# Kernel optimization log

Measured on AMD Instinct MI355X. Metric: run time of the kernel, lower is better.

The kernel has to match this reference:

```python
import jax, jax.numpy as jnp
import numpy as np

H = 12      # num_attention_heads
DM = 768    # hidden_size
HD = DM // H  # head_dim = 64


def setup_inputs() -> dict:
    key = jax.random.key(0)
    ks = jax.random.split(key, 9)
    B, L = 4, 2048
    s = 0.02
    return {
        "hidden_states": jax.random.normal(ks[0], (B, L, DM), jnp.float32),
        "wq": jax.random.normal(ks[1], (DM, DM), jnp.float32) * s,
        "bq": jnp.zeros((DM,), jnp.float32),
        "wk": jax.random.normal(ks[2], (DM, DM), jnp.float32) * s,
        "bk": jnp.zeros((DM,), jnp.float32),
        "wv": jax.random.normal(ks[3], (DM, DM), jnp.float32) * s,
        "bv": jnp.zeros((DM,), jnp.float32),
        "wo": jax.random.normal(ks[4], (DM, DM), jnp.float32) * s,
        "bo": jnp.zeros((DM,), jnp.float32),
    }


def reference(hidden_states, wq, bq, wk, bk, wv, bv, wo, bo):
    B, L, D = hidden_states.shape
    scale = HD ** -0.5
    # torch Linear: x @ W.T + b
    q = hidden_states @ wq.T + bq
    k = hidden_states @ wk.T + bk
    v = hidden_states @ wv.T + bv
    # [B, H, L, HD]
    q = q.reshape(B, L, H, HD).transpose(0, 2, 1, 3)
    k = k.reshape(B, L, H, HD).transpose(0, 2, 1, 3)
    v = v.reshape(B, L, H, HD).transpose(0, 2, 1, 3)
    attn = jnp.einsum('bhqd,bhkd->bhqk', q, k) * scale
    causal = jnp.tril(jnp.ones((L, L), dtype=bool))
    attn = jnp.where(causal, attn, jnp.float32(-jnp.inf))
    attn = jax.nn.softmax(attn, axis=-1)
    out = jnp.einsum('bhqk,bhkd->bhqd', attn, v)
    out = out.transpose(0, 2, 1, 3).reshape(B, L, D)
    return out @ wo.T + bo
```

## Files before the change

kernel.cpp:

```cpp
#include <hip/hip_runtime.h>

typedef unsigned short ushort_t;
typedef __attribute__((ext_vector_type(8))) short short8;
typedef __attribute__((ext_vector_type(4))) float f32x4;

__device__ __forceinline__ ushort_t f2b(float f) {
    union { float f; unsigned int i; } v; v.f = f;
    unsigned int x = v.i;
    return (ushort_t)((x + 0x7fffu + ((x >> 16) & 1u)) >> 16);
}
__device__ __forceinline__ ushort_t f2b_fast(float f) {
    union { float f; unsigned int i; } v; v.f = f;
    return (ushort_t)((v.i + 0x8000u) >> 16);
}
__device__ __forceinline__ float exp2_hw(float x) {
    return __builtin_amdgcn_exp2f(x);
}
__device__ __forceinline__ void dma16(const ushort_t* g, ushort_t* l) {
    __builtin_amdgcn_global_load_lds(
        (const __attribute__((address_space(1))) unsigned int*)g,
        (__attribute__((address_space(3))) unsigned int*)l, 16, 0, 0);
}

__global__ __launch_bounds__(256)
void convert_bf16(const float* __restrict__ hs, const float* __restrict__ wq,
                  const float* __restrict__ wk, const float* __restrict__ wv,
                  const float* __restrict__ wo,
                  ushort_t* __restrict__ hsb, ushort_t* __restrict__ wqb,
                  ushort_t* __restrict__ wkb, ushort_t* __restrict__ wvb,
                  ushort_t* __restrict__ wob)
{
    const int y = blockIdx.y;
    const float* src; ushort_t* dst; int n;
    if (y == 0)      { src = hs; dst = hsb; n = 8192 * 768; }
    else if (y == 1) { src = wq; dst = wqb; n = 768 * 768; }
    else if (y == 2) { src = wk; dst = wkb; n = 768 * 768; }
    else if (y == 3) { src = wv; dst = wvb; n = 768 * 768; }
    else             { src = wo; dst = wob; n = 768 * 768; }
    const int idx = (blockIdx.x * 256 + threadIdx.x) * 8;
    if (idx >= n) return;
    const float4 a = ((const float4*)(src + idx))[0];
    const float4 b = ((const float4*)(src + idx))[1];
    ushort_t tmp[8] = { f2b(a.x), f2b(a.y), f2b(a.z), f2b(a.w),
                        f2b(b.x), f2b(b.y), f2b(b.z), f2b(b.w) };
    *(uint4*)(dst + idx) = *(const uint4*)tmp;
}

#define NIT 24

template<int MODE>
__global__ __launch_bounds__(256, 3)
void gemm_mfma(const ushort_t* __restrict__ A,
               const ushort_t* __restrict__ W0, const ushort_t* __restrict__ W1,
               const ushort_t* __restrict__ W2,
               const float* __restrict__ b0, const float* __restrict__ b1,
               const float* __restrict__ b2,
               void* __restrict__ C0, void* __restrict__ C1, void* __restrict__ C2)
{
    __shared__ __attribute__((aligned(16))) ushort_t Ab[3][128 * 32];
    __shared__ __attribute__((aligned(16))) ushort_t Wb[3][128 * 32];

    const int id   = blockIdx.x;
    const int xcd  = id & 7;
    const int slot = id >> 3;
    int mtile, otile, z;
    if (MODE == 0) {
        mtile = (slot / 18) * 8 + xcd;
        const int rem = slot % 18;
        otile = rem % 6;
        z     = rem / 6;
    } else {
        mtile = (slot / 6) * 8 + xcd;
        otile = slot % 6;
        z     = 0;
    }
    const ushort_t* W = (z == 0) ? W0 : (z == 1) ? W1 : W2;
    const float* bias  = (z == 0) ? b0 : (z == 1) ? b1 : b2;
    void* C            = (z == 0) ? C0 : (z == 1) ? C1 : C2;

    const int t    = threadIdx.x;
    const int lane = t & 63;
    const int w    = t >> 6;
    const int col  = lane & 15;
    const int kg   = lane >> 4;
    const int m0   = mtile * 128;
    const int o0   = otile * 128;
    const int mh   = (w & 1) * 64;
    const int oh   = (w >> 1) * 64;

    f32x4 acc[4][4];
#pragma unroll
    for (int mt = 0; mt < 4; ++mt)
#pragma unroll
        for (int nt = 0; nt < 4; ++nt) acc[mt][nt] = (f32x4){0.f, 0.f, 0.f, 0.f};

    const int lrow = lane >> 2;
    const int lgr  = (lane & 3) ^ ((lane >> 3) & 3);
    const ushort_t* pa = A + (size_t)(m0 + lrow) * 768 + lgr * 8;
    const ushort_t* pw = W + (size_t)(o0 + lrow) * 768 + lgr * 8;

    auto stage = [&](int c, int b) {
#pragma unroll
        for (int j = 0; j < 2; ++j) {
            const int q = 2 * w + j;
            dma16(pa + (size_t)q * (16 * 768) + c * 32, &Ab[b][q * 512]);
            dma16(pw + (size_t)q * (16 * 768) + c * 32, &Wb[b][q * 512]);
        }
    };

    const int gq = (kg ^ ((col >> 1) & 3)) * 8;

    auto step = [&](int it, int cur, int nb) {
        __builtin_amdgcn_s_barrier();
        if (it + 2 < NIT) {
            stage(it + 2, nb);
            asm volatile("s_waitcnt vmcnt(8)" ::: "memory");
        } else if (it + 1 < NIT) {
            asm volatile("s_waitcnt vmcnt(4)" ::: "memory");
        } else {
            asm volatile("s_waitcnt vmcnt(0)" ::: "memory");
        }
        __builtin_amdgcn_sched_barrier(0);

        short8 wf[4], af[4];
#pragma unroll
        for (int nt = 0; nt < 4; ++nt)
            wf[nt] = *(const short8*)&Wb[cur][(oh + nt * 16 + col) * 32 + gq];
#pragma unroll
        for (int mt = 0; mt < 4; ++mt)
            af[mt] = *(const short8*)&Ab[cur][(mh + mt * 16 + col) * 32 + gq];

#pragma unroll
        for (int mt = 0; mt < 4; ++mt)
#pragma unroll
            for (int nt = 0; nt < 4; ++nt)
                acc[mt][nt] = __builtin_amdgcn_mfma_f32_16x16x32_bf16(
                    af[mt], wf[nt], acc[mt][nt], 0, 0, 0);
    };

    stage(0, 0);
    stage(1, 1);
    for (int j = 0; j < NIT; j += 3) {
        step(j + 0, 0, 2);
        step(j + 1, 1, 0);
        step(j + 2, 2, 1);
    }

    float bias_v[4];
#pragma unroll
    for (int nt = 0; nt < 4; ++nt) bias_v[nt] = bias[o0 + oh + nt * 16 + col];
    const float scale = (MODE == 0 && z == 0) ? 0.18033688011112042f : 1.0f;

#pragma unroll
    for (int mt = 0; mt < 4; ++mt)
#pragma unroll
        for (int nt = 0; nt < 4; ++nt) {
            const int mb = m0 + mh + mt * 16 + kg * 4;
            const int o  = o0 + oh + nt * 16 + col;
            if (MODE == 0 && z == 2) {
                ushort_t tmp[4];
#pragma unroll
                for (int r = 0; r < 4; ++r) tmp[r] = f2b(acc[mt][nt][r] + bias_v[nt]);
                const size_t dst = ((size_t)((mb >> 11) * 12 + (o >> 6)) << 17)
                                 + ((size_t)(o & 63) << 11) + (mb & 2047);
                *(uint2*)((ushort_t*)C + dst) = *(const uint2*)tmp;
            } else {
#pragma unroll
                for (int r = 0; r < 4; ++r) {
                    const int m = mb + r;
                    const float v = (acc[mt][nt][r] + bias_v[nt]) * scale;
                    if (MODE == 0) {
                        const size_t dst = ((size_t)((m >> 11) * 12 + (o >> 6)) << 17)
                                         + ((size_t)(m & 2047) << 6) + (o & 63);
                        ((ushort_t*)C)[dst] = f2b(v);
                    } else {
                        ((float*)C)[(size_t)m * 768 + o] = v;
                    }
                }
            }
        }
}

#define KV_STRIDE 72

__global__ __launch_bounds__(256, 3)
void attn_mfma(const ushort_t* __restrict__ Q, const ushort_t* __restrict__ K,
               const ushort_t* __restrict__ Vt, ushort_t* __restrict__ AO)
{
    __shared__ ushort_t Ks[64 * KV_STRIDE];
    __shared__ ushort_t Vs[64 * KV_STRIDE];

    const int t    = threadIdx.x;
    const int lane = t & 63;
    const int w    = t >> 6;
    const int id   = blockIdx.x;
    const int bh   = ((id >> 3) >> 4) * 8 + (id & 7);
    const int p    = (id >> 3) & 15;
    const size_t base = (size_t)bh << 17;

    const int col = lane & 15;
    const int kg  = lane >> 4;
    const int srow = t >> 2;
    const int scol = (t & 3) << 4;
    const int b = bh / 12, h = bh % 12;

#pragma unroll
    for (int phase = 0; phase < 2; ++phase) {
        const int tile = phase ? p : (31 - p);
        const int q0   = tile << 6;
        const int nch  = tile + 1;

        const ushort_t* pq = Q + base + (size_t)(q0 + 16 * w + col) * 64 + kg * 8;
        const short8 bq0 = *(const short8*)pq;
        const short8 bq1 = *(const short8*)(pq + 32);

        const int qcur = q0 + 16 * w + col;

        float l_run = 0.f;
        f32x4 o_acc[4];
#pragma unroll
        for (int vt = 0; vt < 4; ++vt) o_acc[vt] = (f32x4){0.f, 0.f, 0.f, 0.f};

        uint4 ka, kb, va, vb;
        {
            const ushort_t* pk = K  + base + (size_t)srow * 64 + scol;
            const ushort_t* pv = Vt + base + ((size_t)srow << 11) + scol;
            ka = *(const uint4*)pk; kb = *(const uint4*)(pk + 8);
            va = *(const uint4*)pv; vb = *(const uint4*)(pv + 8);
        }

        for (int c = 0; c < nch; ++c) {
            __syncthreads();
            *(uint4*)&Ks[srow * KV_STRIDE + scol]     = ka;
            *(uint4*)&Ks[srow * KV_STRIDE + scol + 8] = kb;
            *(uint4*)&Vs[srow * KV_STRIDE + scol]     = va;
            *(uint4*)&Vs[srow * KV_STRIDE + scol + 8] = vb;
            __syncthreads();

            if (c + 1 < nch) {
                const int k1 = (c + 1) << 6;
                const ushort_t* pk = K  + base + (size_t)(k1 + srow) * 64 + scol;
                const ushort_t* pv = Vt + base + ((size_t)srow << 11) + k1 + scol;
                ka = *(const uint4*)pk; kb = *(const uint4*)(pk + 8);
                va = *(const uint4*)pv; vb = *(const uint4*)(pv + 8);
            }

            f32x4 s[4];
            __builtin_amdgcn_s_setprio(1);
#pragma unroll
            for (int kt = 0; kt < 4; ++kt) {
                const ushort_t* pkf = &Ks[(kt * 16 + col) * KV_STRIDE + kg * 8];
                const short8 ak0 = *(const short8*)pkf;
                const short8 ak1 = *(const short8*)(pkf + 32);
                f32x4 acc = (f32x4){0.f, 0.f, 0.f, 0.f};
                acc = __builtin_amdgcn_mfma_f32_16x16x32_bf16(ak0, bq0, acc, 0, 0, 0);
                acc = __builtin_amdgcn_mfma_f32_16x16x32_bf16(ak1, bq1, acc, 0, 0, 0);
                s[kt] = acc;
            }
            __builtin_amdgcn_s_setprio(0);

            if (c == nch - 1) {
                const int k0 = c << 6;
#pragma unroll
                for (int kt = 0; kt < 4; ++kt)
#pragma unroll
                    for (int r = 0; r < 4; ++r) {
                        const int key = k0 + kt * 16 + 4 * kg + r;
                        s[kt][r] = (key > qcur) ? 0.f : exp2_hw(s[kt][r]);
                    }
            } else {
#pragma unroll
                for (int kt = 0; kt < 4; ++kt)
#pragma unroll
                    for (int r = 0; r < 4; ++r) s[kt][r] = exp2_hw(s[kt][r]);
            }
#pragma unroll
            for (int kt = 0; kt < 4; ++kt)
                l_run += (s[kt][0] + s[kt][1]) + (s[kt][2] + s[kt][3]);

            unsigned int P2[4][2];
#pragma unroll
            for (int kt = 0; kt < 4; ++kt) {
                asm("v_cvt_pk_bf16_f32 %0, %1, %2"
                    : "=v"(P2[kt][0]) : "v"(s[kt][0]), "v"(s[kt][1]));
                asm("v_cvt_pk_bf16_f32 %0, %1, %2"
                    : "=v"(P2[kt][1]) : "v"(s[kt][2]), "v"(s[kt][3]));
            }
            const bool klo = (kg < 2);
            unsigned int X16[4], X32[4];
            X16[0] = klo ? P2[0][0] : P2[1][0];
            X16[1] = klo ? P2[0][1] : P2[1][1];
            X16[2] = klo ? P2[2][0] : P2[3][0];
            X16[3] = klo ? P2[2][1] : P2[3][1];
            X32[0] = klo ? P2[1][0] : P2[0][0];
            X32[1] = klo ? P2[1][1] : P2[0][1];
            X32[2] = klo ? P2[3][0] : P2[2][0];
            X32[3] = klo ? P2[3][1] : P2[2][1];
            unsigned int R16[4], R32[4], R48[4];
#pragma unroll
            for (int j = 0; j < 4; ++j) {
                R16[j] = (unsigned int)__shfl_xor((int)X16[j], 16);
                R32[j] = (unsigned int)__shfl_xor((int)X32[j], 32);
                R48[j] = (unsigned int)__shfl_xor((int)X32[j], 48);
            }
            unsigned int Fv[4], Sv[4];
#pragma unroll
            for (int j = 0; j < 4; ++j) {
                const unsigned int flo = (kg == 0) ? X16[j] : R48[j];
                const unsigned int fhi = (kg == 2) ? R32[j] : R16[j];
                Fv[j] = klo ? flo : fhi;
                const unsigned int slo = (kg == 0) ? R16[j] : R32[j];
                const unsigned int shi = (kg == 2) ? R48[j] : X16[j];
                Sv[j] = klo ? slo : shi;
            }
            union { unsigned int u[4]; short8 v; } A0, A1;
            A0.u[0] = Fv[0]; A0.u[1] = Fv[1]; A0.u[2] = Sv[0]; A0.u[3] = Sv[1];
            A1.u[0] = Fv[2]; A1.u[1] = Fv[3]; A1.u[2] = Sv[2]; A1.u[3] = Sv[3];
            const short8 pa0 = A0.v;
            const short8 pa1 = A1.v;

            __builtin_amdgcn_s_setprio(1);
#pragma unroll
            for (int vt = 0; vt < 4; ++vt) {
                const ushort_t* pvf = &Vs[(vt * 16 + col) * KV_STRIDE + kg * 8];
                const short8 v0 = *(const short8*)pvf;
                const short8 v1 = *(const short8*)(pvf + 32);
                f32x4 o = o_acc[vt];
                o = __builtin_amdgcn_mfma_f32_16x16x32_bf16(pa0, v0, o, 0, 0, 0);
                o = __builtin_amdgcn_mfma_f32_16x16x32_bf16(pa1, v1, o, 0, 0, 0);
                o_acc[vt] = o;
            }
            __builtin_amdgcn_s_setprio(0);
        }

        float ls = l_run;
        ls += __shfl_xor(ls, 16);
        ls += __shfl_xor(ls, 32);
        const float linv = 1.f / ls;
        float linv4[4];
#pragma unroll
        for (int r = 0; r < 4; ++r)
            linv4[r] = __shfl(linv, 4 * kg + r);
#pragma unroll
        for (int vt = 0; vt < 4; ++vt)
#pragma unroll
            for (int r = 0; r < 4; ++r) {
                const int q = q0 + 16 * w + 4 * kg + r;
                AO[((size_t)(b * 2048 + q)) * 768 + h * 64 + vt * 16 + col] =
                    f2b_fast(o_acc[vt][r] * linv4[r]);
            }
    }
}

extern "C" void kernel_launch(void* const* d_in, const int* in_sizes, int n_in,
                              void* d_out, int out_size, void* d_ws, size_t ws_size,
                              hipStream_t stream) {
    const float* hs = (const float*)d_in[0];
    const float* wq = (const float*)d_in[1];
    const float* bq = (const float*)d_in[2];
    const float* wk = (const float*)d_in[3];
    const float* bk = (const float*)d_in[4];
    const float* wv = (const float*)d_in[5];
    const float* bv = (const float*)d_in[6];
    const float* wo = (const float*)d_in[7];
    const float* bo = (const float*)d_in[8];
    float* out = (float*)d_out;

    const size_t NB = (size_t)8192 * 768;
    const size_t WN = (size_t)768 * 768;
    ushort_t* hsb = (ushort_t*)d_ws;
    ushort_t* Qb  = hsb + NB;
    ushort_t* Kb  = Qb + NB;
    ushort_t* Vtb = Kb + NB;
    ushort_t* wqb = Vtb + NB;
    ushort_t* wkb = wqb + WN;
    ushort_t* wvb = wkb + WN;
    ushort_t* wob = wvb + WN;
    ushort_t* AO  = hsb;

    dim3 blk(256);
    convert_bf16<<<dim3(3072, 5), blk, 0, stream>>>(hs, wq, wk, wv, wo,
                                                    hsb, wqb, wkb, wvb, wob);
    gemm_mfma<0><<<dim3(1152), blk, 0, stream>>>(hsb, wqb, wkb, wvb,
                                                 bq, bk, bv, Qb, Kb, Vtb);
    attn_mfma<<<dim3(768), blk, 0, stream>>>(Qb, Kb, Vtb, AO);
    gemm_mfma<1><<<dim3(384), blk, 0, stream>>>(AO, wob, wob, wob,
                                                bo, bo, bo, out, out, out);
}
```

Baseline: 208.9 us.

## Fuse paired causal query tiles into one KV pass sharing K/V loads

Each workgroup previously handled two query tiles (31-p and p) in two sequential phases, streaming K/V separately for each. Now both tiles share a single KV loop: each K/V chunk staged in LDS is used for tile A always and for tile B while the chunk index is at most p. This cuts global K/V loads and LDS staging and barriers by up to about a third, and gives the scheduler two independent MFMA chains to interleave. The cost is more live registers (two Q fragments, two sets of accumulators and scores) under launch_bounds(256,3), which may cause spills, plus a branch on doB.

Measured after the change: 209.1 us. About the same (+0.1%).

```diff
diff --git a/kernel.cpp b/kernel.cpp
--- a/kernel.cpp
+++ b/kernel.cpp
@@ -183,6 +183,53 @@
 
 #define KV_STRIDE 72
 
+struct pafrag { short8 a0, a1; };
+
+__device__ __forceinline__ pafrag p_redist(f32x4 s0, f32x4 s1, f32x4 s2,
+                                           f32x4 s3, int kg)
+{
+    unsigned int P2[4][2];
+    asm("v_cvt_pk_bf16_f32 %0, %1, %2" : "=v"(P2[0][0]) : "v"(s0[0]), "v"(s0[1]));
+    asm("v_cvt_pk_bf16_f32 %0, %1, %2" : "=v"(P2[0][1]) : "v"(s0[2]), "v"(s0[3]));
+    asm("v_cvt_pk_bf16_f32 %0, %1, %2" : "=v"(P2[1][0]) : "v"(s1[0]), "v"(s1[1]));
+    asm("v_cvt_pk_bf16_f32 %0, %1, %2" : "=v"(P2[1][1]) : "v"(s1[2]), "v"(s1[3]));
+    asm("v_cvt_pk_bf16_f32 %0, %1, %2" : "=v"(P2[2][0]) : "v"(s2[0]), "v"(s2[1]));
+    asm("v_cvt_pk_bf16_f32 %0, %1, %2" : "=v"(P2[2][1]) : "v"(s2[2]), "v"(s2[3]));
+    asm("v_cvt_pk_bf16_f32 %0, %1, %2" : "=v"(P2[3][0]) : "v"(s3[0]), "v"(s3[1]));
+    asm("v_cvt_pk_bf16_f32 %0, %1, %2" : "=v"(P2[3][1]) : "v"(s3[2]), "v"(s3[3]));
+    const bool klo = (kg < 2);
+    unsigned int X16[4], X32[4];
+    X16[0] = klo ? P2[0][0] : P2[1][0];
+    X16[1] = klo ? P2[0][1] : P2[1][1];
+    X16[2] = klo ? P2[2][0] : P2[3][0];
+    X16[3] = klo ? P2[2][1] : P2[3][1];
+    X32[0] = klo ? P2[1][0] : P2[0][0];
+    X32[1] = klo ? P2[1][1] : P2[0][1];
+    X32[2] = klo ? P2[3][0] : P2[2][0];
+    X32[3] = klo ? P2[3][1] : P2[2][1];
+    unsigned int R16[4], R32[4], R48[4];
+#pragma unroll
+    for (int j = 0; j < 4; ++j) {
+        R16[j] = (unsigned int)__shfl_xor((int)X16[j], 16);
+        R32[j] = (unsigned int)__shfl_xor((int)X32[j], 32);
+        R48[j] = (unsigned int)__shfl_xor((int)X32[j], 48);
+    }
+    unsigned int Fv[4], Sv[4];
+#pragma unroll
+    for (int j = 0; j < 4; ++j) {
+        const unsigned int flo = (kg == 0) ? X16[j] : R48[j];
+        const unsigned int fhi = (kg == 2) ? R32[j] : R16[j];
+        Fv[j] = klo ? flo : fhi;
+        const unsigned int slo = (kg == 0) ? R16[j] : R32[j];
+        const unsigned int shi = (kg == 2) ? R48[j] : X16[j];
+        Sv[j] = klo ? slo : shi;
+    }
+    union { unsigned int u[4]; short8 v; } A0, A1;
+    A0.u[0] = Fv[0]; A0.u[1] = Fv[1]; A0.u[2] = Sv[0]; A0.u[3] = Sv[1];
+    A1.u[0] = Fv[2]; A1.u[1] = Fv[3]; A1.u[2] = Sv[2]; A1.u[3] = Sv[3];
+    pafrag r; r.a0 = A0.v; r.a1 = A1.v; return r;
+}
+
 __global__ __launch_bounds__(256, 3)
 void attn_mfma(const ushort_t* __restrict__ Q, const ushort_t* __restrict__ K,
                const ushort_t* __restrict__ Vt, ushort_t* __restrict__ AO)
@@ -204,152 +251,161 @@
     const int scol = (t & 3) << 4;
     const int b = bh / 12, h = bh % 12;
 
-#pragma unroll
-    for (int phase = 0; phase < 2; ++phase) {
-        const int tile = phase ? p : (31 - p);
-        const int q0   = tile << 6;
-        const int nch  = tile + 1;
-
-        const ushort_t* pq = Q + base + (size_t)(q0 + 16 * w + col) * 64 + kg * 8;
-        const short8 bq0 = *(const short8*)pq;
-        const short8 bq1 = *(const short8*)(pq + 32);
-
-        const int qcur = q0 + 16 * w + col;
-
-        float l_run = 0.f;
-        f32x4 o_acc[4];
-#pragma unroll
-        for (int vt = 0; vt < 4; ++vt) o_acc[vt] = (f32x4){0.f, 0.f, 0.f, 0.f};
-
-        uint4 ka, kb, va, vb;
-        {
-            const ushort_t* pk = K  + base + (size_t)srow * 64 + scol;
-            const ushort_t* pv = Vt + base + ((size_t)srow << 11) + scol;
+    const int tileA = 31 - p;
+    const int tileB = p;
+    const int q0A = tileA << 6, q0B = tileB << 6;
+    const int nch = tileA + 1;
+
+    const ushort_t* pqA = Q + base + (size_t)(q0A + 16 * w + col) * 64 + kg * 8;
+    const ushort_t* pqB = Q + base + (size_t)(q0B + 16 * w + col) * 64 + kg * 8;
+    const short8 bqA0 = *(const short8*)pqA;
+    const short8 bqA1 = *(const short8*)(pqA + 32);
+    const short8 bqB0 = *(const short8*)pqB;
+    const short8 bqB1 = *(const short8*)(pqB + 32);
+
+    const int qcurA = q0A + 16 * w + col;
+    const int qcurB = q0B + 16 * w + col;
+
+    float l_runA = 0.f, l_runB = 0.f;
+    f32x4 oA[4], oB[4];
+#pragma unroll
+    for (int vt = 0; vt < 4; ++vt) {
+        oA[vt] = (f32x4){0.f, 0.f, 0.f, 0.f};
+        oB[vt] = (f32x4){0.f, 0.f, 0.f, 0.f};
+    }
+
+    uint4 ka, kb, va, vb;
+    {
+        const ushort_t* pk = K  + base + (size_t)srow * 64 + scol;
+        const ushort_t* pv = Vt + base + ((size_t)srow << 11) + scol;
+        ka = *(const uint4*)pk; kb = *(const uint4*)(pk + 8);
+        va = *(const uint4*)pv; vb = *(const uint4*)(pv + 8);
+    }
+
+    for (int c = 0; c < nch; ++c) {
+        __syncthreads();
+        *(uint4*)&Ks[srow * KV_STRIDE + scol]     = ka;
+        *(uint4*)&Ks[srow * KV_STRIDE + scol + 8] = kb;
+        *(uint4*)&Vs[srow * KV_STRIDE + scol]     = va;
+        *(uint4*)&Vs[srow * KV_STRIDE + scol + 8] = vb;
+        __syncthreads();
+
+        if (c + 1 < nch) {
+            const int k1 = (c + 1) << 6;
+            const ushort_t* pk = K  + base + (size_t)(k1 + srow) * 64 + scol;
+            const ushort_t* pv = Vt + base + ((size_t)srow << 11) + k1 + scol;
             ka = *(const uint4*)pk; kb = *(const uint4*)(pk + 8);
             va = *(const uint4*)pv; vb = *(const uint4*)(pv + 8);
         }
 
-        for (int c = 0; c < nch; ++c) {
-            __syncthreads();
-            *(uint4*)&Ks[srow * KV_STRIDE + scol]     = ka;
-            *(uint4*)&Ks[srow * KV_STRIDE + scol + 8] = kb;
-            *(uint4*)&Vs[srow * KV_STRIDE + scol]     = va;
-            *(uint4*)&Vs[srow * KV_STRIDE + scol + 8] = vb;
-            __syncthreads();
-
-            if (c + 1 < nch) {
-                const int k1 = (c + 1) << 6;
-                const ushort_t* pk = K  + base + (size_t)(k1 + srow) * 64 + scol;
-                const ushort_t* pv = Vt + base + ((size_t)srow << 11) + k1 + scol;
-                ka = *(const uint4*)pk; kb = *(const uint4*)(pk + 8);
-                va = *(const uint4*)pv; vb = *(const uint4*)(pv + 8);
+        const bool doB = (c <= tileB);
+
+        f32x4 sA[4], sB[4];
+        __builtin_amdgcn_s_setprio(1);
+#pragma unroll
+        for (int kt = 0; kt < 4; ++kt) {
+            const ushort_t* pkf = &Ks[(kt * 16 + col) * KV_STRIDE + kg * 8];
+            const short8 ak0 = *(const short8*)pkf;
+            const short8 ak1 = *(const short8*)(pkf + 32);
+            f32x4 a = (f32x4){0.f, 0.f, 0.f, 0.f};
+            a = __builtin_amdgcn_mfma_f32_16x16x32_bf16(ak0, bqA0, a, 0, 0, 0);
+            a = __builtin_amdgcn_mfma_f32_16x16x32_bf16(ak1, bqA1, a, 0, 0, 0);
+            sA[kt] = a;
+            if (doB) {
+                f32x4 bb = (f32x4){0.f, 0.f, 0.f, 0.f};
+                bb = __builtin_amdgcn_mfma_f32_16x16x32_bf16(ak0, bqB0, bb, 0, 0, 0);
+                bb = __builtin_amdgcn_mfma_f32_16x16x32_bf16(ak1, bqB1, bb, 0, 0, 0);
+                sB[kt] = bb;
             }
-
-            f32x4 s[4];
-            __builtin_amdgcn_s_setprio(1);
-#pragma unroll
-            for (int kt = 0; kt < 4; ++kt) {
-                const ushort_t* pkf = &Ks[(kt * 16 + col) * KV_STRIDE + kg * 8];
-                const short8 ak0 = *(const short8*)pkf;
-                const short8 ak1 = *(const short8*)(pkf + 32);
-                f32x4 acc = (f32x4){0.f, 0.f, 0.f, 0.f};
-                acc = __builtin_amdgcn_mfma_f32_16x16x32_bf16(ak0, bq0, acc, 0, 0, 0);
-                acc = __builtin_amdgcn_mfma_f32_16x16x32_bf16(ak1, bq1, acc, 0, 0, 0);
-                s[kt] = acc;
-            }
-            __builtin_amdgcn_s_setprio(0);
-
-            if (c == nch - 1) {
+        }
+        __builtin_amdgcn_s_setprio(0);
+
+        if (c == nch - 1) {
+            const int k0 = c << 6;
+#pragma unroll
+            for (int kt = 0; kt < 4; ++kt)
+#pragma unroll
+                for (int r = 0; r < 4; ++r) {
+                    const int key = k0 + kt * 16 + 4 * kg + r;
+                    sA[kt][r] = (key > qcurA) ? 0.f : exp2_hw(sA[kt][r]);
+                }
+        } else {
+#pragma unroll
+            for (int kt = 0; kt < 4; ++kt)
+#pragma unroll
+                for (int r = 0; r < 4; ++r) sA[kt][r] = exp2_hw(sA[kt][r]);
+        }
+#pragma unroll
+        for (int kt = 0; kt < 4; ++kt)
+            l_runA += (sA[kt][0] + sA[kt][1]) + (sA[kt][2] + sA[kt][3]);
+
+        if (doB) {
+            if (c == tileB) {
                 const int k0 = c << 6;
 #pragma unroll
                 for (int kt = 0; kt < 4; ++kt)
 #pragma unroll
                     for (int r = 0; r < 4; ++r) {
                         const int key = k0 + kt * 16 + 4 * kg + r;
-                        s[kt][r] = (key > qcur) ? 0.f : exp2_hw(s[kt][r]);
+                        sB[kt][r] = (key > qcurB) ? 0.f : exp2_hw(sB[kt][r]);
                     }
             } else {
 #pragma unroll
                 for (int kt = 0; kt < 4; ++kt)
 #pragma unroll
-                    for (int r = 0; r < 4; ++r) s[kt][r] = exp2_hw(s[kt][r]);
+                    for (int r = 0; r < 4; ++r) sB[kt][r] = exp2_hw(sB[kt][r]);
             }
 #pragma unroll
             for (int kt = 0; kt < 4; ++kt)
-                l_run += (s[kt][0] + s[kt][1]) + (s[kt][2] + s[kt][3]);
-
-            unsigned int P2[4][2];
-#pragma unroll
-            for (int kt = 0; kt < 4; ++kt) {
-                asm("v_cvt_pk_bf16_f32 %0, %1, %2"
-                    : "=v"(P2[kt][0]) : "v"(s[kt][0]), "v"(s[kt][1]));
-                asm("v_cvt_pk_bf16_f32 %0, %1, %2"
-                    : "=v"(P2[kt][1]) : "v"(s[kt][2]), "v"(s[kt][3]));
+                l_runB += (sB[kt][0] + sB[kt][1]) + (sB[kt][2] + sB[kt][3]);
+        }
+
+        pafrag pA = p_redist(sA[0], sA[1], sA[2], sA[3], kg);
+        pafrag pB;
+        if (doB) pB = p_redist(sB[0], sB[1], sB[2], sB[3], kg);
+
+        __builtin_amdgcn_s_setprio(1);
+#pragma unroll
+        for (int vt = 0; vt < 4; ++vt) {
+            const ushort_t* pvf = &Vs[(vt * 16 + col) * KV_STRIDE + kg * 8];
+            const short8 v0 = *(const short8*)pvf;
+            const short8 v1 = *(const short8*)(pvf + 32);
+            f32x4 o = oA[vt];
+            o = __builtin_amdgcn_mfma_f32_16x16x32_bf16(pA.a0, v0, o, 0, 0, 0);
+            o = __builtin_amdgcn_mfma_f32_16x16x32_bf16(pA.a1, v1, o, 0, 0, 0);
+            oA[vt] = o;
+            if (doB) {
+                f32x4 ob = oB[vt];
+                ob = __builtin_amdgcn_mfma_f32_16x16x32_bf16(pB.a0, v0, ob, 0, 0, 0);
+                ob = __builtin_amdgcn_mfma_f32_16x16x32_bf16(pB.a1, v1, ob, 0, 0, 0);
+                oB[vt] = ob;
             }
-            const bool klo = (kg < 2);
-            unsigned int X16[4], X32[4];
-            X16[0] = klo ? P2[0][0] : P2[1][0];
-            X16[1] = klo ? P2[0][1] : P2[1][1];
-            X16[2] = klo ? P2[2][0] : P2[3][0];
-            X16[3] = klo ? P2[2][1] : P2[3][1];
-            X32[0] = klo ? P2[1][0] : P2[0][0];
-            X32[1] = klo ? P2[1][1] : P2[0][1];
-            X32[2] = klo ? P2[3][0] : P2[2][0];
-            X32[3] = klo ? P2[3][1] : P2[2][1];
-            unsigned int R16[4], R32[4], R48[4];
-#pragma unroll
-            for (int j = 0; j < 4; ++j) {
-                R16[j] = (unsigned int)__shfl_xor((int)X16[j], 16);
-                R32[j] = (unsigned int)__shfl_xor((int)X32[j], 32);
-                R48[j] = (unsigned int)__shfl_xor((int)X32[j], 48);
-            }
-            unsigned int Fv[4], Sv[4];
-#pragma unroll
-            for (int j = 0; j < 4; ++j) {
-                const unsigned int flo = (kg == 0) ? X16[j] : R48[j];
-                const unsigned int fhi = (kg == 2) ? R32[j] : R16[j];
-                Fv[j] = klo ? flo : fhi;
-                const unsigned int slo = (kg == 0) ? R16[j] : R32[j];
-                const unsigned int shi = (kg == 2) ? R48[j] : X16[j];
-                Sv[j] = klo ? slo : shi;
-            }
-            union { unsigned int u[4]; short8 v; } A0, A1;
-            A0.u[0] = Fv[0]; A0.u[1] = Fv[1]; A0.u[2] = Sv[0]; A0.u[3] = Sv[1];
-            A1.u[0] = Fv[2]; A1.u[1] = Fv[3]; A1.u[2] = Sv[2]; A1.u[3] = Sv[3];
-            const short8 pa0 = A0.v;
-            const short8 pa1 = A1.v;
-
-            __builtin_amdgcn_s_setprio(1);
-#pragma unroll
-            for (int vt = 0; vt < 4; ++vt) {
-                const ushort_t* pvf = &Vs[(vt * 16 + col) * KV_STRIDE + kg * 8];
-                const short8 v0 = *(const short8*)pvf;
-                const short8 v1 = *(const short8*)(pvf + 32);
-                f32x4 o = o_acc[vt];
-                o = __builtin_amdgcn_mfma_f32_16x16x32_bf16(pa0, v0, o, 0, 0, 0);
-                o = __builtin_amdgcn_mfma_f32_16x16x32_bf16(pa1, v1, o, 0, 0, 0);
-                o_acc[vt] = o;
-            }
-            __builtin_amdgcn_s_setprio(0);
-        }
-
-        float ls = l_run;
-        ls += __shfl_xor(ls, 16);
-        ls += __shfl_xor(ls, 32);
-        const float linv = 1.f / ls;
-        float linv4[4];
-#pragma unroll
-        for (int r = 0; r < 4; ++r)
-            linv4[r] = __shfl(linv, 4 * kg + r);
-#pragma unroll
-        for (int vt = 0; vt < 4; ++vt)
-#pragma unroll
-            for (int r = 0; r < 4; ++r) {
-                const int q = q0 + 16 * w + 4 * kg + r;
-                AO[((size_t)(b * 2048 + q)) * 768 + h * 64 + vt * 16 + col] =
-                    f2b_fast(o_acc[vt][r] * linv4[r]);
-            }
-    }
+        }
+        __builtin_amdgcn_s_setprio(0);
+    }
+
+    float lsA = l_runA, lsB = l_runB;
+    lsA += __shfl_xor(lsA, 16); lsA += __shfl_xor(lsA, 32);
+    lsB += __shfl_xor(lsB, 16); lsB += __shfl_xor(lsB, 32);
+    const float linvA = 1.f / lsA;
+    const float linvB = 1.f / lsB;
+    float lA4[4], lB4[4];
+#pragma unroll
+    for (int r = 0; r < 4; ++r) {
+        lA4[r] = __shfl(linvA, 4 * kg + r);
+        lB4[r] = __shfl(linvB, 4 * kg + r);
+    }
+#pragma unroll
+    for (int vt = 0; vt < 4; ++vt)
+#pragma unroll
+        for (int r = 0; r < 4; ++r) {
+            const int qA = q0A + 16 * w + 4 * kg + r;
+            const int qB = q0B + 16 * w + 4 * kg + r;
+            AO[((size_t)(b * 2048 + qA)) * 768 + h * 64 + vt * 16 + col] =
+                f2b_fast(oA[vt][r] * lA4[r]);
+            AO[((size_t)(b * 2048 + qB)) * 768 + h * 64 + vt * 16 + col] =
+                f2b_fast(oB[vt][r] * lB4[r]);
+        }
 }
 
 extern "C" void kernel_launch(void* const* d_in, const int* in_sizes, int n_in,
```
